# Performance work log

Hardware: AMD Instinct MI355X
Metric: run time of the kernel (lower is better)

## Reference

```python
import jax, jax.numpy as jnp
import numpy as np

N_EMBDS = 1024
N_HEADS = 16
HEAD_DIM = N_EMBDS // N_HEADS


def setup_inputs() -> dict:
    key = jax.random.key(0)
    ks = jax.random.split(key, 5)
    B, T, C = 2, 2048, N_EMBDS
    x = jax.random.normal(ks[0], (B, T, C), dtype=jnp.float32)
    s = 1.0 / np.sqrt(C)
    W_attn = jax.random.normal(ks[1], (C, 3 * C), dtype=jnp.float32) * s
    b_attn = jnp.zeros((3 * C,), dtype=jnp.float32)
    W_proj = jax.random.normal(ks[2], (C, C), dtype=jnp.float32) * s
    b_proj = jnp.zeros((C,), dtype=jnp.float32)
    return {"x": x, "W_attn": W_attn, "b_attn": b_attn, "W_proj": W_proj, "b_proj": b_proj}


def reference(x, W_attn, b_attn, W_proj, b_proj):
    B, T, C = x.shape
    H, D = N_HEADS, HEAD_DIM
    qkv = x @ W_attn + b_attn  # [B, T, 3C]
    q, k, v = jnp.split(qkv, 3, axis=-1)
    # [B, H, T, D]
    q = q.reshape(B, T, H, D).transpose(0, 2, 1, 3)
    k = k.reshape(B, T, H, D).transpose(0, 2, 1, 3)
    v = v.reshape(B, T, H, D).transpose(0, 2, 1, 3)
    att = jnp.einsum('bhqd,bhkd->bhqk', q, k) * (1.0 / np.sqrt(D))  # [B,H,T,T]
    causal = jnp.tril(jnp.ones((T, T), dtype=bool))
    att = jnp.where(causal[None, None], att, -jnp.inf)
    att = jax.nn.softmax(att, axis=-1)
    y = jnp.einsum('bhqk,bhkd->bhqd', att, v)  # [B,H,T,D]
    y = y.transpose(0, 2, 1, 3).reshape(B, T, C)
    return y @ W_proj + b_proj
```

## Files before the change

### kernel.cpp

```cpp
#include <hip/hip_runtime.h>
#include <hip/hip_bf16.h>


typedef __bf16 bf16x8 __attribute__((ext_vector_type(8)));
typedef float  f32x4  __attribute__((ext_vector_type(4)));
#define BF16 __hip_bfloat16

constexpr int Bb = 2, Tt = 2048, Cc = 1024, Hh = 16, Dd = 64;
constexpr float NEG_INF = -1e30f;

__device__ __forceinline__ f32x4 mfma16(bf16x8 a, bf16x8 b, f32x4 c) {
  return __builtin_amdgcn_mfma_f32_16x16x32_bf16(a, b, c, 0, 0, 0);
}

__device__ __forceinline__ void gll16(const void* g, void* l) {
  __builtin_amdgcn_global_load_lds((const __attribute__((address_space(1))) void*)g,
                                   (__attribute__((address_space(3))) void*)l,
                                   16, 0, 0);
}

__device__ __forceinline__ int swz64(int r, int c) {
  return r * 64 + ((((c >> 3) ^ r) & 7) << 3) + (c & 7);
}

__device__ __forceinline__ int kperm(int kr) {
  return (((kr >> 5) << 1) + ((kr >> 2) & 1)) * 16 + (((kr >> 3) & 3) << 2) + (kr & 3);
}

__global__ void prep_kernel(const float* __restrict__ x, BF16* __restrict__ xb,
                            const float* __restrict__ Wa, BF16* __restrict__ WaT,
                            const float* __restrict__ Wp, BF16* __restrict__ WpT) {
  __shared__ float tile[32][33];
  const int bx = blockIdx.x, tid = threadIdx.x;
  if (bx < 2048) {
    const int i = (bx * 256 + tid) * 8;
    const float4 a = *(const float4*)&x[i];
    const float4 b = *(const float4*)&x[i + 4];
    BF16 o[8];
    o[0] = __float2bfloat16(a.x); o[1] = __float2bfloat16(a.y);
    o[2] = __float2bfloat16(a.z); o[3] = __float2bfloat16(a.w);
    o[4] = __float2bfloat16(b.x); o[5] = __float2bfloat16(b.y);
    o[6] = __float2bfloat16(b.z); o[7] = __float2bfloat16(b.w);
    *(uint4*)&xb[i] = *(const uint4*)o;
    return;
  }
  const float* in; BF16* outT; int K, N, gx, gy;
  if (bx < 5120) {
    const int idx = bx - 2048;
    in = Wa; outT = WaT; K = 1024; N = 3072; gx = idx % 96; gy = idx / 96;
  } else {
    const int idx = bx - 5120;
    in = Wp; outT = WpT; K = 1024; N = 1024; gx = idx % 32; gy = idx / 32;
  }
  const int n0 = gx * 32, k0 = gy * 32;
  const int tx = tid & 31, ty = tid >> 5;
#pragma unroll
  for (int i = ty; i < 32; i += 8) tile[i][tx] = in[(size_t)(k0 + i) * N + (n0 + tx)];
  __syncthreads();
#pragma unroll
  for (int i = ty; i < 32; i += 8)
    outT[(size_t)(n0 + i) * K + (k0 + tx)] = __float2bfloat16(tile[tx][i]);
}

template <int MODE>
__global__ __launch_bounds__(256) void gemm_bt(const BF16* __restrict__ A,
                                               const BF16* __restrict__ Bt,
                                               const float* __restrict__ bias,
                                               BF16* __restrict__ oq,
                                               BF16* __restrict__ ok,
                                               BF16* __restrict__ ov,
                                               float* __restrict__ fout,
                                               int Ndim, int Kdim) {
  __shared__ alignas(16) BF16 sA[128 * 32];
  __shared__ alignas(16) BF16 sB[128 * 32];
  const int tid = threadIdx.x;
  const int wave = tid >> 6, lane = tid & 63;
  const int quad = lane >> 4, l16 = lane & 15;
  const int wm = (wave >> 1) * 64, wn = (wave & 1) * 64;
  const int bm = blockIdx.y * 128, bn = blockIdx.x * 128;

  f32x4 acc[4][4];
#pragma unroll
  for (int i = 0; i < 4; ++i)
#pragma unroll
    for (int j = 0; j < 4; ++j) acc[i][j] = f32x4{0.f, 0.f, 0.f, 0.f};

  const int rowA = wave * 32 + (lane >> 2);
  const int sub8 = (lane & 3) * 8;
  const BF16* gA0 = &A[(size_t)(bm + rowA) * Kdim + sub8];
  const BF16* gB0 = &Bt[(size_t)(bn + rowA) * Kdim + sub8];
  const size_t rstep16 = (size_t)16 * Kdim;
  BF16* lA0 = &sA[wave * 1024];
  BF16* lA1 = &sA[wave * 1024 + 512];
  BF16* lB0 = &sB[wave * 1024];
  BF16* lB1 = &sB[wave * 1024 + 512];

  for (int k0 = 0; k0 < Kdim; k0 += 32) {
    __syncthreads();
    gll16(gA0 + k0, lA0);
    gll16(gA0 + rstep16 + k0, lA1);
    gll16(gB0 + k0, lB0);
    gll16(gB0 + rstep16 + k0, lB1);
    __syncthreads();

    bf16x8 af[4], bf_[4];
#pragma unroll
    for (int i = 0; i < 4; ++i)
      af[i] = *(const bf16x8*)&sA[(wm + i * 16 + l16) * 32 + quad * 8];
#pragma unroll
    for (int j = 0; j < 4; ++j)
      bf_[j] = *(const bf16x8*)&sB[(wn + j * 16 + l16) * 32 + quad * 8];
#pragma unroll
    for (int i = 0; i < 4; ++i)
#pragma unroll
      for (int j = 0; j < 4; ++j) acc[i][j] = mfma16(af[i], bf_[j], acc[i][j]);
  }

#pragma unroll
  for (int j = 0; j < 4; ++j) {
    const int gn = bn + wn + j * 16 + l16;
    const float bsv = bias[gn];
    if (MODE == 1) {
#pragma unroll
      for (int i = 0; i < 4; ++i)
#pragma unroll
        for (int r = 0; r < 4; ++r) {
          const int gm = bm + wm + i * 16 + quad * 4 + r;
          fout[(size_t)gm * Ndim + gn] = acc[i][j][r] + bsv;
        }
    } else {
      const int which = (bn + wn + j * 16) >> 10;
      const int c = gn & 1023;
      const int hh = c >> 6, dd = c & 63;
#pragma unroll
      for (int i = 0; i < 4; ++i) {
        const int gm0 = bm + wm + i * 16 + quad * 4;
        const int bb = gm0 >> 11, tk0 = gm0 & 2047;
        const size_t bh = (size_t)(bb * Hh + hh);
        if (which == 2) {
          BF16 tmp[4];
#pragma unroll
          for (int r = 0; r < 4; ++r) tmp[r] = __float2bfloat16(acc[i][j][r] + bsv);
          *(uint2*)&ov[(bh * Dd + dd) * Tt + tk0] = *(const uint2*)tmp;
        } else {
          BF16* dst = (which == 0) ? oq : ok;
          const float scale = (which == 0) ? 0.125f : 1.0f;
#pragma unroll
          for (int r = 0; r < 4; ++r)
            dst[(bh * Tt + tk0 + r) * Dd + dd] =
                __float2bfloat16((acc[i][j][r] + bsv) * scale);
        }
      }
    }
  }
}

__global__ __launch_bounds__(256) void attn_kernel(const BF16* __restrict__ qg,
                                                   const BF16* __restrict__ kg,
                                                   const BF16* __restrict__ vtg,
                                                   BF16* __restrict__ yb) {
  __shared__ alignas(16) BF16 sK[2 * 64 * 64];
  __shared__ alignas(16) BF16 sV[2 * 64 * 64];
  const int pr = blockIdx.x, h = blockIdx.y, b = blockIdx.z;
  const int tid = threadIdx.x;
  const int wave = tid >> 6, lane = tid & 63;
  const int quad = lane >> 4, l16 = lane & 15;
  const int qs = (wave >> 1) ? (63 - pr) : pr;
  const int sub = wave & 1;
  const int jt_diag = qs >> 1;
  const int jt_max = (63 - pr) >> 1;
  const size_t base = ((size_t)(b * Hh + h)) * Tt * Dd;
  const int qrow0 = qs * 32 + sub * 16;

  bf16x8 qf0, qf1;
  {
    const size_t off = base + (size_t)(qrow0 + l16) * Dd;
    qf0 = *(const bf16x8*)&qg[off + quad * 8];
    qf1 = *(const bf16x8*)&qg[off + 32 + quad * 8];
  }

  bf16x8 ones8;
#pragma unroll
  for (int j = 0; j < 8; ++j) ones8[j] = (__bf16)1.0f;

  f32x4 o[4], oL;
#pragma unroll
  for (int i = 0; i < 4; ++i) o[i] = f32x4{0.f, 0.f, 0.f, 0.f};
  oL = f32x4{0.f, 0.f, 0.f, 0.f};

  const int krow = tid >> 2, kcg = (tid & 3) * 16;
  const int kprow = kperm(krow);
  const int wK0 = swz64(kprow, kcg), wK1 = swz64(kprow, kcg + 8);
  const int wV0 = swz64(krow, kcg), wV1 = swz64(krow, kcg + 8);

  uint4 rk0, rk1, rv0, rv1;
  {
    const uint4* pk = (const uint4*)&kg[base + (size_t)krow * Dd + kcg];
    const uint4* pv = (const uint4*)&vtg[base + (size_t)krow * Tt + kcg];
    rk0 = pk[0]; rk1 = pk[1];
    rv0 = pv[0]; rv1 = pv[1];
  }

  for (int jt = 0; jt <= jt_max; ++jt) {
    BF16* sKb = &sK[(jt & 1) * 4096];
    BF16* sVb = &sV[(jt & 1) * 4096];
    *(uint4*)&sKb[wK0] = rk0;
    *(uint4*)&sKb[wK1] = rk1;
    *(uint4*)&sVb[wV0] = rv0;
    *(uint4*)&sVb[wV1] = rv1;
    if (jt < jt_max) {
      const int kb2 = (jt + 1) * 64;
      const uint4* nk = (const uint4*)&kg[base + (size_t)(kb2 + krow) * Dd + kcg];
      const uint4* nv = (const uint4*)&vtg[base + (size_t)krow * Tt + kb2 + kcg];
      rk0 = nk[0]; rk1 = nk[1];
      rv0 = nv[0]; rv1 = nv[1];
    }
    __syncthreads();

    if (jt > jt_diag) continue;
    const int kb = jt * 64;

    f32x4 sS[4];
    __builtin_amdgcn_s_setprio(1);
#pragma unroll
    for (int t = 0; t < 4; ++t) {
      const bf16x8 kf0 = *(const bf16x8*)&sKb[swz64(t * 16 + l16, quad * 8)];
      const bf16x8 kf1 = *(const bf16x8*)&sKb[swz64(t * 16 + l16, 32 + quad * 8)];
      sS[t] = mfma16(kf0, qf0, f32x4{0.f, 0.f, 0.f, 0.f});
      sS[t] = mfma16(kf1, qf1, sS[t]);
    }
    __builtin_amdgcn_s_setprio(0);

    if (jt == jt_diag) {
      const int q = qrow0 + l16;
#pragma unroll
      for (int t = 0; t < 4; ++t) {
        const int kc0 = kb + (t >> 1) * 32 + quad * 8 + (t & 1) * 4;
#pragma unroll
        for (int r = 0; r < 4; ++r)
          if (kc0 + r > q) sS[t][r] = NEG_INF;
      }
    }

    bf16x8 pf[2];
#pragma unroll
    for (int cc = 0; cc < 2; ++cc)
#pragma unroll
      for (int j = 0; j < 8; ++j)
        pf[cc][j] = (__bf16)__expf(sS[cc * 2 + (j >> 2)][j & 3] - 12.0f);

    __builtin_amdgcn_s_setprio(1);
#pragma unroll
    for (int cc = 0; cc < 2; ++cc) {
#pragma unroll
      for (int dt = 0; dt < 4; ++dt) {
        const bf16x8 vb =
            *(const bf16x8*)&sVb[swz64(dt * 16 + l16, cc * 32 + quad * 8)];
        o[dt] = mfma16(pf[cc], vb, o[dt]);
      }
      oL = mfma16(pf[cc], ones8, oL);
    }
    __builtin_amdgcn_s_setprio(0);
  }

#pragma unroll
  for (int r = 0; r < 4; ++r) {
    const float inv = 1.0f / oL[r];
    const int trow = qrow0 + quad * 4 + r;
#pragma unroll
    for (int dt = 0; dt < 4; ++dt)
      yb[((size_t)(b * Tt + trow)) * Cc + h * Dd + dt * 16 + l16] =
          __float2bfloat16(o[dt][r] * inv);
  }
}

extern "C" void kernel_launch(void* const* d_in, const int* in_sizes, int n_in,
                              void* d_out, int out_size, void* d_ws, size_t ws_size,
                              hipStream_t stream) {
  (void)in_sizes; (void)n_in; (void)out_size; (void)ws_size;
  const float* x      = (const float*)d_in[0];
  const float* W_attn = (const float*)d_in[1];
  const float* b_attn = (const float*)d_in[2];
  const float* W_proj = (const float*)d_in[3];
  const float* b_proj = (const float*)d_in[4];
  float* out = (float*)d_out;

  constexpr size_t SZ_WA = (size_t)3072 * 1024;
  constexpr size_t SZ_WP = (size_t)1024 * 1024;
  constexpr size_t SZ_X  = (size_t)4096 * 1024;
  constexpr size_t SZ_T  = (size_t)Bb * Hh * Tt * Dd;

  BF16* ws   = (BF16*)d_ws;
  BF16* wtAb = ws;
  BF16* wtPb = wtAb + SZ_WA;
  BF16* xb   = wtPb + SZ_WP;
  BF16* q    = xb + SZ_X;
  BF16* k    = q + SZ_T;
  BF16* vt   = k + SZ_T;
  BF16* yb   = vt + SZ_T;

  prep_kernel<<<dim3(6144), 256, 0, stream>>>(x, xb, W_attn, wtAb, W_proj, wtPb);
  gemm_bt<0><<<dim3(24, 32), 256, 0, stream>>>(xb, wtAb, b_attn, q, k, vt, nullptr,
                                               3072, 1024);
  attn_kernel<<<dim3(32, 16, 2), 256, 0, stream>>>(q, k, vt, yb);
  gemm_bt<1><<<dim3(8, 32), 256, 0, stream>>>(yb, wtPb, b_proj, nullptr, nullptr,
                                              nullptr, out, 1024, 1024);
}
```

Before: 189.7 us.

## Replace QKV GEMM with 256x256-tile double-buffered 8-wave kernel

Adds a dedicated QKV projection GEMM that uses 256x256 block tiles, 8 waves and a 64-wide K step. Operands are staged with direct global-to-LDS loads into double-buffered, XOR-swizzled shared memory, and the loads for the next K chunk are interleaved with MFMA compute under wave priority hints. This cuts global traffic per FLOP and overlaps loads with math, aiming to speed up the largest GEMM. The cost is 128KB of LDS per block and only 192 blocks, which may underfill the GPU's 256 CUs. The old templated GEMM is reduced to the output-projection path only.

After: 197.3 us. 1.04x slower.

```diff
diff --git a/kernel.cpp b/kernel.cpp
--- a/kernel.cpp
+++ b/kernel.cpp
@@ -62,13 +62,161 @@
     outT[(size_t)(n0 + i) * K + (k0 + tx)] = __float2bfloat16(tile[tx][i]);
 }
 
+__global__ __launch_bounds__(512, 2) void gemm256_qkv(const BF16* __restrict__ A,
+                                                      const BF16* __restrict__ Bt,
+                                                      const float* __restrict__ bias,
+                                                      BF16* __restrict__ oq,
+                                                      BF16* __restrict__ ok,
+                                                      BF16* __restrict__ ov) {
+  __shared__ alignas(16) BF16 sAs[2][16384];
+  __shared__ alignas(16) BF16 sBs[2][16384];
+  const int tid = threadIdx.x;
+  const int wave = tid >> 6, lane = tid & 63;
+  const int quad = lane >> 4, l16 = lane & 15;
+  const int wr = wave >> 2, wc = wave & 3;
+  const int wr128 = wr * 128, wc64 = wc * 64;
+  const int bm = blockIdx.y * 256, bn = blockIdx.x * 256;
+  const int sw = l16 & 7;
+
+  const int srow = tid >> 3;
+  const int sgl = (tid & 7) ^ (srow & 7);
+  const BF16* gA = &A[(size_t)(bm + srow) * 1024 + sgl * 8];
+  const BF16* gB = &Bt[(size_t)(bn + srow) * 1024 + sgl * 8];
+
+#define STAGE_A(b, c, kc) \
+  gll16(gA + (size_t)(c) * 64 * 1024 + (kc), &sAs[b][(c) * 4096 + wave * 512])
+#define STAGE_B(b, c, kc) \
+  gll16(gB + (size_t)(c) * 64 * 1024 + (kc), &sBs[b][(c) * 4096 + wave * 512])
+
+  f32x4 acc[8][4];
+#pragma unroll
+  for (int m = 0; m < 8; ++m)
+#pragma unroll
+    for (int n = 0; n < 4; ++n) acc[m][n] = f32x4{0.f, 0.f, 0.f, 0.f};
+
+  STAGE_A(0, 0, 0); STAGE_A(0, 2, 0);
+  STAGE_B(0, 0, 0); STAGE_B(0, 1, 0); STAGE_B(0, 2, 0); STAGE_B(0, 3, 0);
+  STAGE_A(0, 1, 0); STAGE_A(0, 3, 0);
+
+  for (int t = 0; t < 16; ++t) {
+    const int cur = t & 1, nxt = cur ^ 1;
+    const int kc = ((t + 1) & 15) * 64;
+    const BF16* sAc = sAs[cur];
+    const BF16* sBc = sBs[cur];
+
+    asm volatile("s_waitcnt vmcnt(2)" ::: "memory");
+    __builtin_amdgcn_s_barrier();
+    asm volatile("" ::: "memory");
+
+    STAGE_A(nxt, 0, kc); STAGE_A(nxt, 2, kc);
+    bf16x8 af[4][2], bfa[2][2], bfb[2][2];
+#pragma unroll
+    for (int m = 0; m < 4; ++m)
+#pragma unroll
+      for (int h = 0; h < 2; ++h)
+        af[m][h] = *(const bf16x8*)
+            &sAc[(wr128 + m * 16 + l16) * 64 + (((h * 4 + quad) ^ sw) << 3)];
+#pragma unroll
+    for (int n = 0; n < 2; ++n)
+#pragma unroll
+      for (int h = 0; h < 2; ++h)
+        bfa[n][h] = *(const bf16x8*)
+            &sBc[(wc64 + n * 16 + l16) * 64 + (((h * 4 + quad) ^ sw) << 3)];
+    __builtin_amdgcn_s_setprio(1);
+#pragma unroll
+    for (int m = 0; m < 4; ++m)
+#pragma unroll
+      for (int n = 0; n < 2; ++n) {
+        acc[m][n] = mfma16(af[m][0], bfa[n][0], acc[m][n]);
+        acc[m][n] = mfma16(af[m][1], bfa[n][1], acc[m][n]);
+      }
+    __builtin_amdgcn_s_setprio(0);
+
+    STAGE_B(nxt, 0, kc); STAGE_B(nxt, 1, kc);
+#pragma unroll
+    for (int n = 0; n < 2; ++n)
+#pragma unroll
+      for (int h = 0; h < 2; ++h)
+        bfb[n][h] = *(const bf16x8*)
+            &sBc[(wc64 + 32 + n * 16 + l16) * 64 + (((h * 4 + quad) ^ sw) << 3)];
+    __builtin_amdgcn_s_setprio(1);
+#pragma unroll
+    for (int m = 0; m < 4; ++m)
+#pragma unroll
+      for (int n = 0; n < 2; ++n) {
+        acc[m][2 + n] = mfma16(af[m][0], bfb[n][0], acc[m][2 + n]);
+        acc[m][2 + n] = mfma16(af[m][1], bfb[n][1], acc[m][2 + n]);
+      }
+    __builtin_amdgcn_s_setprio(0);
+
+    asm volatile("s_waitcnt vmcnt(4)" ::: "memory");
+    __builtin_amdgcn_s_barrier();
+    asm volatile("" ::: "memory");
+
+    STAGE_B(nxt, 2, kc); STAGE_B(nxt, 3, kc);
+#pragma unroll
+    for (int m = 0; m < 4; ++m)
+#pragma unroll
+      for (int h = 0; h < 2; ++h)
+        af[m][h] = *(const bf16x8*)
+            &sAc[(wr128 + 64 + m * 16 + l16) * 64 + (((h * 4 + quad) ^ sw) << 3)];
+    __builtin_amdgcn_s_setprio(1);
+#pragma unroll
+    for (int m = 0; m < 4; ++m)
+#pragma unroll
+      for (int n = 0; n < 2; ++n) {
+        acc[4 + m][n] = mfma16(af[m][0], bfa[n][0], acc[4 + m][n]);
+        acc[4 + m][n] = mfma16(af[m][1], bfa[n][1], acc[4 + m][n]);
+      }
+    __builtin_amdgcn_s_setprio(0);
+
+    STAGE_A(nxt, 1, kc); STAGE_A(nxt, 3, kc);
+    __builtin_amdgcn_s_setprio(1);
+#pragma unroll
+    for (int m = 0; m < 4; ++m)
+#pragma unroll
+      for (int n = 0; n < 2; ++n) {
+        acc[4 + m][2 + n] = mfma16(af[m][0], bfb[n][0], acc[4 + m][2 + n]);
+        acc[4 + m][2 + n] = mfma16(af[m][1], bfb[n][1], acc[4 + m][2 + n]);
+      }
+    __builtin_amdgcn_s_setprio(0);
+  }
+#undef STAGE_A
+#undef STAGE_B
+
+#pragma unroll
+  for (int n = 0; n < 4; ++n) {
+    const int gn = bn + wc64 + n * 16 + l16;
+    const float bsv = bias[gn];
+    const int which = (bn + wc64 + n * 16) >> 10;
+    const int c = gn & 1023;
+    const int hh = c >> 6, dd = c & 63;
+#pragma unroll
+    for (int m = 0; m < 8; ++m) {
+      const int gm0 = bm + wr128 + m * 16 + quad * 4;
+      const int bb = gm0 >> 11, tk0 = gm0 & 2047;
+      const size_t bh = (size_t)(bb * Hh + hh);
+      if (which == 2) {
+        BF16 tmp[4];
+#pragma unroll
+        for (int r = 0; r < 4; ++r) tmp[r] = __float2bfloat16(acc[m][n][r] + bsv);
+        *(uint2*)&ov[(bh * Dd + dd) * Tt + tk0] = *(const uint2*)tmp;
+      } else {
+        BF16* dst = (which == 0) ? oq : ok;
+        const float scale = (which == 0) ? 0.125f : 1.0f;
+#pragma unroll
+        for (int r = 0; r < 4; ++r)
+          dst[(bh * Tt + tk0 + r) * Dd + dd] =
+              __float2bfloat16((acc[m][n][r] + bsv) * scale);
+      }
+    }
+  }
+}
+
 template <int MODE>
 __global__ __launch_bounds__(256) void gemm_bt(const BF16* __restrict__ A,
                                                const BF16* __restrict__ Bt,
                                                const float* __restrict__ bias,
-                                               BF16* __restrict__ oq,
-                                               BF16* __restrict__ ok,
-                                               BF16* __restrict__ ov,
                                                float* __restrict__ fout,
                                                int Ndim, int Kdim) {
   __shared__ alignas(16) BF16 sA[128 * 32];
@@ -120,38 +268,13 @@
   for (int j = 0; j < 4; ++j) {
     const int gn = bn + wn + j * 16 + l16;
     const float bsv = bias[gn];
-    if (MODE == 1) {
-#pragma unroll
-      for (int i = 0; i < 4; ++i)
-#pragma unroll
-        for (int r = 0; r < 4; ++r) {
-          const int gm = bm + wm + i * 16 + quad * 4 + r;
-          fout[(size_t)gm * Ndim + gn] = acc[i][j][r] + bsv;
-        }
-    } else {
-      const int which = (bn + wn + j * 16) >> 10;
-      const int c = gn & 1023;
-      const int hh = c >> 6, dd = c & 63;
-#pragma unroll
-      for (int i = 0; i < 4; ++i) {
-        const int gm0 = bm + wm + i * 16 + quad * 4;
-        const int bb = gm0 >> 11, tk0 = gm0 & 2047;
-        const size_t bh = (size_t)(bb * Hh + hh);
-        if (which == 2) {
-          BF16 tmp[4];
-#pragma unroll
-          for (int r = 0; r < 4; ++r) tmp[r] = __float2bfloat16(acc[i][j][r] + bsv);
-          *(uint2*)&ov[(bh * Dd + dd) * Tt + tk0] = *(const uint2*)tmp;
-        } else {
-          BF16* dst = (which == 0) ? oq : ok;
-          const float scale = (which == 0) ? 0.125f : 1.0f;
-#pragma unroll
-          for (int r = 0; r < 4; ++r)
-            dst[(bh * Tt + tk0 + r) * Dd + dd] =
-                __float2bfloat16((acc[i][j][r] + bsv) * scale);
-        }
-      }
-    }
+#pragma unroll
+    for (int i = 0; i < 4; ++i)
+#pragma unroll
+      for (int r = 0; r < 4; ++r) {
+        const int gm = bm + wm + i * 16 + quad * 4 + r;
+        fout[(size_t)gm * Ndim + gn] = acc[i][j][r] + bsv;
+      }
   }
 }
 
@@ -300,9 +423,7 @@
   BF16* yb   = vt + SZ_T;
 
   prep_kernel<<<dim3(6144), 256, 0, stream>>>(x, xb, W_attn, wtAb, W_proj, wtPb);
-  gemm_bt<0><<<dim3(24, 32), 256, 0, stream>>>(xb, wtAb, b_attn, q, k, vt, nullptr,
-                                               3072, 1024);
+  gemm256_qkv<<<dim3(12, 16), 512, 0, stream>>>(xb, wtAb, b_attn, q, k, vt);
   attn_kernel<<<dim3(32, 16, 2), 256, 0, stream>>>(q, k, vt, yb);
-  gemm_bt<1><<<dim3(8, 32), 256, 0, stream>>>(yb, wtPb, b_proj, nullptr, nullptr,
-                                              nullptr, out, 1024, 1024);
-}
+  gemm_bt<1><<<dim3(8, 32), 256, 0, stream>>>(yb, wtPb, b_proj, out, 1024, 1024);
+}
```

## Double GEMM K-tile to 64 with XOR-swizzled LDS and remap attention blocks

Applied to the files above, without the earlier changes.

The GEMM now stages a 64-wide K slice per iteration instead of 32, which halves the number of barrier pairs per K loop. Each row's 16-byte chunks are stored with an XOR swizzle so the MFMA fragment reads avoid LDS bank conflicts. The attention launch becomes a 1D grid, with block IDs permuted so that consecutive blocks land on different XCDs, spreading heads and batches across chiplets for cache locality. LDS use per GEMM block doubles, which could reduce occupancy.

Result: faster. 182.2 us (-4.0%).

```diff
diff --git a/kernel.cpp b/kernel.cpp
--- a/kernel.cpp
+++ b/kernel.cpp
@@ -71,13 +71,14 @@
                                                BF16* __restrict__ ov,
                                                float* __restrict__ fout,
                                                int Ndim, int Kdim) {
-  __shared__ alignas(16) BF16 sA[128 * 32];
-  __shared__ alignas(16) BF16 sB[128 * 32];
+  __shared__ alignas(16) BF16 sA[128 * 64];
+  __shared__ alignas(16) BF16 sB[128 * 64];
   const int tid = threadIdx.x;
   const int wave = tid >> 6, lane = tid & 63;
   const int quad = lane >> 4, l16 = lane & 15;
   const int wm = (wave >> 1) * 64, wn = (wave & 1) * 64;
   const int bm = blockIdx.y * 128, bn = blockIdx.x * 128;
+  const int sw = l16 & 7;
 
   f32x4 acc[4][4];
 #pragma unroll
@@ -85,35 +86,37 @@
 #pragma unroll
     for (int j = 0; j < 4; ++j) acc[i][j] = f32x4{0.f, 0.f, 0.f, 0.f};
 
-  const int rowA = wave * 32 + (lane >> 2);
-  const int sub8 = (lane & 3) * 8;
-  const BF16* gA0 = &A[(size_t)(bm + rowA) * Kdim + sub8];
-  const BF16* gB0 = &Bt[(size_t)(bn + rowA) * Kdim + sub8];
-  const size_t rstep16 = (size_t)16 * Kdim;
-  BF16* lA0 = &sA[wave * 1024];
-  BF16* lA1 = &sA[wave * 1024 + 512];
-  BF16* lB0 = &sB[wave * 1024];
-  BF16* lB1 = &sB[wave * 1024 + 512];
-
-  for (int k0 = 0; k0 < Kdim; k0 += 32) {
+  const int srow = wave * 32 + (lane >> 3);
+  const int sgl = (lane ^ (lane >> 3)) & 7;
+  const BF16* gA0 = &A[(size_t)(bm + srow) * Kdim + sgl * 8];
+  const BF16* gB0 = &Bt[(size_t)(bn + srow) * Kdim + sgl * 8];
+  const size_t rstep8 = (size_t)8 * Kdim;
+
+  for (int k0 = 0; k0 < Kdim; k0 += 64) {
     __syncthreads();
-    gll16(gA0 + k0, lA0);
-    gll16(gA0 + rstep16 + k0, lA1);
-    gll16(gB0 + k0, lB0);
-    gll16(gB0 + rstep16 + k0, lB1);
+#pragma unroll
+    for (int s = 0; s < 4; ++s) {
+      gll16(gA0 + s * rstep8 + k0, &sA[wave * 2048 + s * 512]);
+      gll16(gB0 + s * rstep8 + k0, &sB[wave * 2048 + s * 512]);
+    }
     __syncthreads();
 
-    bf16x8 af[4], bf_[4];
-#pragma unroll
-    for (int i = 0; i < 4; ++i)
-      af[i] = *(const bf16x8*)&sA[(wm + i * 16 + l16) * 32 + quad * 8];
-#pragma unroll
-    for (int j = 0; j < 4; ++j)
-      bf_[j] = *(const bf16x8*)&sB[(wn + j * 16 + l16) * 32 + quad * 8];
-#pragma unroll
-    for (int i = 0; i < 4; ++i)
-#pragma unroll
-      for (int j = 0; j < 4; ++j) acc[i][j] = mfma16(af[i], bf_[j], acc[i][j]);
+#pragma unroll
+    for (int h = 0; h < 2; ++h) {
+      bf16x8 af[4], bf_[4];
+#pragma unroll
+      for (int i = 0; i < 4; ++i)
+        af[i] = *(const bf16x8*)
+            &sA[(wm + i * 16 + l16) * 64 + (((h * 4 + quad) ^ sw) << 3)];
+#pragma unroll
+      for (int j = 0; j < 4; ++j)
+        bf_[j] = *(const bf16x8*)
+            &sB[(wn + j * 16 + l16) * 64 + (((h * 4 + quad) ^ sw) << 3)];
+#pragma unroll
+      for (int i = 0; i < 4; ++i)
+#pragma unroll
+        for (int j = 0; j < 4; ++j) acc[i][j] = mfma16(af[i], bf_[j], acc[i][j]);
+    }
   }
 
 #pragma unroll
@@ -161,7 +164,9 @@
                                                    BF16* __restrict__ yb) {
   __shared__ alignas(16) BF16 sK[2 * 64 * 64];
   __shared__ alignas(16) BF16 sV[2 * 64 * 64];
-  const int pr = blockIdx.x, h = blockIdx.y, b = blockIdx.z;
+  const int id = blockIdx.x;
+  const int swz = ((id & 7) << 7) + (id >> 3);
+  const int pr = swz & 31, h = (swz >> 5) & 15, b = swz >> 9;
   const int tid = threadIdx.x;
   const int wave = tid >> 6, lane = tid & 63;
   const int quad = lane >> 4, l16 = lane & 15;
@@ -302,7 +307,7 @@
   prep_kernel<<<dim3(6144), 256, 0, stream>>>(x, xb, W_attn, wtAb, W_proj, wtPb);
   gemm_bt<0><<<dim3(24, 32), 256, 0, stream>>>(xb, wtAb, b_attn, q, k, vt, nullptr,
                                                3072, 1024);
-  attn_kernel<<<dim3(32, 16, 2), 256, 0, stream>>>(q, k, vt, yb);
+  attn_kernel<<<dim3(1024), 256, 0, stream>>>(q, k, vt, yb);
   gemm_bt<1><<<dim3(8, 32), 256, 0, stream>>>(yb, wtPb, b_proj, nullptr, nullptr,
                                               nullptr, out, 1024, 1024);
 }
```
